# Kernel tuning notes

Measured on AMD Instinct MI355X. Metric: run time of the kernel, lower is better.

## Reference

```python
import jax, jax.numpy as jnp
import numpy as np

B, N, D, H = 4, 2048, 512, 8
KD = D // H  # per-head key/value dim = 64
NORM = 1.0 / np.sqrt(KD).astype(np.float32)


def setup_inputs() -> dict:
    key = jax.random.key(0)
    kq, km, k1, k2, k3 = jax.random.split(key, 5)
    s = 1.0 / np.sqrt(D)
    return {
        "queries": jax.random.normal(kq, (B, N, D), dtype=jnp.float32),
        "mask": jax.random.randint(km, (B, N, N), 0, 2).astype(jnp.bool_),
        "Wq": jax.random.normal(k1, (D, D), dtype=jnp.float32) * s,
        "Wk": jax.random.normal(k2, (D, D), dtype=jnp.float32) * s,
        "Wc": jax.random.normal(k3, (D, D), dtype=jnp.float32) * s,
    }


def reference(queries, mask, Wq, Wk, Wc):
    # Self-attention path (keys=None, values=None): V uses key_embed (Wk).
    Q = (queries @ Wq.T).reshape(B, N, H, KD)  # [B,N,H,kd]
    K = (queries @ Wk.T).reshape(B, N, H, KD)
    V = K  # original code: V = key_embed(queries) when values is None
    scores = NORM * jnp.einsum("bqhd,bkhd->bhqk", Q, K)  # [B,H,N,N]
    scores = jnp.where(mask[:, None, :, :], -jnp.inf, scores)
    attn = jax.nn.softmax(scores, axis=-1)
    out = jnp.einsum("bhqk,bkhd->bqhd", attn, V).reshape(B, N, H * KD)
    return out @ Wc.T  # [B,N,D]
```

## Files before the change

kernel.cpp:

```cpp
#include <hip/hip_runtime.h>
#include <hip/hip_bf16.h>
#include <math.h>

#define B_ 4
#define N_ 2048
#define D_ 512
#define H_ 8
#define NORM2_ 0.18033688011112042f

typedef __attribute__((ext_vector_type(8))) short short8;
typedef __attribute__((ext_vector_type(4))) float f32x4;
#define MFMA16(a, b, c) __builtin_amdgcn_mfma_f32_16x16x32_bf16(a, b, c, 0, 0, 0)
#define EXP2(x) __builtin_amdgcn_exp2f(x)

static __device__ __forceinline__ uint32_t pk2(float lo, float hi) {
  __hip_bfloat162 h = __float22bfloat162_rn(make_float2(lo, hi));
  return *(reinterpret_cast<uint32_t*>(&h));
}

static __device__ __forceinline__ void async16(const ushort* lds, const ushort* g) {
  __builtin_amdgcn_global_load_lds(
      (const __attribute__((address_space(1))) uint32_t*)g,
      (__attribute__((address_space(3))) uint32_t*)(ushort*)lds, 16, 0, 0);
}

__global__ __launch_bounds__(256) void prep(const float* __restrict__ q,
                                            const int* __restrict__ mask,
                                            const float* __restrict__ wq,
                                            const float* __restrict__ wk,
                                            const float* __restrict__ wc,
                                            ushort* __restrict__ Xb,
                                            ushort* __restrict__ Wb,
                                            uint32_t* __restrict__ pk) {
  const int bx = blockIdx.x;
  if (bx < 2048) {
    const int lane = threadIdx.x & 63;
    const int wid = ((bx << 8) + threadIdx.x) >> 6;
    for (int i = wid; i < 65536; i += 8192) {
      const int4 m = ((const int4*)mask)[(size_t)i * 64 + lane];
      uint32_t nib = (uint32_t)(m.x != 0) | ((uint32_t)(m.y != 0) << 1) |
                     ((uint32_t)(m.z != 0) << 2) | ((uint32_t)(m.w != 0) << 3);
      nib |= __shfl_xor(nib, 1) << 4;
      nib |= __shfl_xor(nib, 2) << 8;
      nib |= __shfl_xor(nib, 4) << 16;
      if ((lane & 7) == 0) pk[i * 8 + (lane >> 3)] = nib;
    }
  } else if (bx < 3072) {
    const int i = ((bx - 2048) << 8) + threadIdx.x;
    for (int j = i; j < 1048576; j += 262144) {
      const float4 v = ((const float4*)q)[j];
      uint2 o; o.x = pk2(v.x, v.y); o.y = pk2(v.z, v.w);
      ((uint2*)Xb)[j] = o;
    }
  } else {
    const int i = ((bx - 3072) << 8) + threadIdx.x;
    for (int j = i; j < 196608; j += 24576) {
      const int wi = j >> 16, off = j & 65535;
      const float* src = (wi == 0) ? wq : (wi == 1) ? wk : wc;
      const float4 v = ((const float4*)src)[off];
      uint2 o; o.x = pk2(v.x, v.y); o.y = pk2(v.z, v.w);
      ((uint2*)Wb)[j] = o;
    }
  }
}

__global__ __launch_bounds__(256) void merge(const ushort* __restrict__ P0,
                                             const float* __restrict__ l0,
                                             const float* __restrict__ l1,
                                             ushort* __restrict__ Ab) {
  const int j = (blockIdx.x << 8) + threadIdx.x;
  const int h = (j >> 3) & 7;
  const int tok = j >> 6;
  const int b = tok >> 11, n = tok & 2047;
  const int li = ((b * H_ + h) << 11) + n;
  const float inv = 1.f / (l0[li] + l1[li]);
  const uint4 a0 = ((const uint4*)P0)[j];
  const uint4 a1 = ((const uint4*)Ab)[j];
  uint4 o;
  const uint32_t* u0 = (const uint32_t*)&a0;
  const uint32_t* u1 = (const uint32_t*)&a1;
  uint32_t* uo = (uint32_t*)&o;
#pragma unroll
  for (int m = 0; m < 4; ++m) {
    const float lo = __uint_as_float(u0[m] << 16) + __uint_as_float(u1[m] << 16);
    const float hi = __uint_as_float(u0[m] & 0xFFFF0000u) +
                     __uint_as_float(u1[m] & 0xFFFF0000u);
    uo[m] = pk2(lo * inv, hi * inv);
  }
  ((uint4*)Ab)[j] = o;
}

template <int F32OUT>
__global__ __launch_bounds__(256) void gemm128(const ushort* __restrict__ X,
                                               const ushort* __restrict__ W0,
                                               const ushort* __restrict__ W1,
                                               void* __restrict__ C0,
                                               void* __restrict__ C1,
                                               float s0, float s1) {
  const ushort* Wp = (blockIdx.z == 0) ? W0 : W1;
  void* Cp = (blockIdx.z == 0) ? C0 : C1;
  const float sc = (blockIdx.z == 0) ? s0 : s1;
  const int t = threadIdx.x;
  const int w = t >> 6, lane = t & 63, quad = lane >> 4, c = lane & 15;
  const int wm = w & 1, wn = w >> 1;
  const int n0 = blockIdx.x * 128, m0 = blockIdx.y * 128;
  __shared__ __align__(16) ushort Xs[2][128][64];
  __shared__ __align__(16) ushort Ws[2][128][64];
  f32x4 acc[4][4];
#pragma unroll
  for (int i = 0; i < 4; ++i)
#pragma unroll
    for (int j = 0; j < 4; ++j) acc[i][j] = (f32x4){0.f, 0.f, 0.f, 0.f};

#define GSTAGE(bf, k0)                                                        \
  do {                                                                        \
    _Pragma("unroll") for (int g = 0; g < 4; ++g) {                           \
      const int id = w * 256 + g * 64 + lane;                                 \
      const int row = id >> 3, lch = id & 7;                                  \
      const int gch = lch ^ (row & 7);                                        \
      async16(&Xs[bf][row][lch * 8], X + (size_t)(m0 + row) * D_ + (k0) + gch * 8); \
      async16(&Ws[bf][row][lch * 8], Wp + (size_t)(n0 + row) * D_ + (k0) + gch * 8); \
    }                                                                         \
  } while (0)

  GSTAGE(0, 0);
  __syncthreads();
  const int NK = D_ / 64;
  for (int kt = 0; kt < NK; ++kt) {
    const int bf = kt & 1;
    if (kt + 1 < NK) GSTAGE(bf ^ 1, (kt + 1) * 64);
#pragma unroll
    for (int s = 0; s < 2; ++s) {
      short8 af[4], bt[4];
#pragma unroll
      for (int i = 0; i < 4; ++i) {
        const int rA = wn * 64 + i * 16 + c;
        af[i] = *(const short8*)&Ws[bf][rA][(((s * 4 + quad) ^ (rA & 7)) & 7) * 8];
        const int rB = wm * 64 + i * 16 + c;
        bt[i] = *(const short8*)&Xs[bf][rB][(((s * 4 + quad) ^ (rB & 7)) & 7) * 8];
      }
#pragma unroll
      for (int i = 0; i < 4; ++i)
#pragma unroll
        for (int j = 0; j < 4; ++j) acc[i][j] = MFMA16(af[i], bt[j], acc[i][j]);
    }
    if (kt + 1 < NK) __syncthreads();
  }
#undef GSTAGE
#pragma unroll
  for (int i = 0; i < 4; ++i)
#pragma unroll
    for (int j = 0; j < 4; ++j) {
      const size_t off =
          (size_t)(m0 + wm * 64 + j * 16 + c) * D_ + n0 + wn * 64 + i * 16 + quad * 4;
      if (F32OUT) {
        float4 v; v.x = acc[i][j][0]; v.y = acc[i][j][1]; v.z = acc[i][j][2]; v.w = acc[i][j][3];
        *(float4*)((float*)Cp + off) = v;
      } else {
        uint2 uv;
        uv.x = pk2(acc[i][j][0] * sc, acc[i][j][1] * sc);
        uv.y = pk2(acc[i][j][2] * sc, acc[i][j][3] * sc);
        *(uint2*)((ushort*)Cp + off) = uv;
      }
    }
}

__global__ __launch_bounds__(256) void attn_mfma(const ushort* __restrict__ Qb,
                                                 const ushort* __restrict__ Kb,
                                                 const uint32_t* __restrict__ pk,
                                                 ushort* __restrict__ P0,
                                                 ushort* __restrict__ P1,
                                                 float* __restrict__ l0,
                                                 float* __restrict__ l1) {
  const int qt64 = blockIdx.x >> 1, hf = blockIdx.x & 1;
  const int h = blockIdx.y, b = blockIdx.z;
  const int q0 = qt64 * 64;
  const int t = threadIdx.x;
  const int w = t >> 6, lane = t & 63, quad = lane >> 4, c = lane & 15;

  __shared__ __align__(16) ushort Ks[64][64];
  __shared__ __align__(16) uint32_t KtU[64][32];
  __shared__ __align__(16) ushort QP[4][16][72];
  ushort(*Qs)[64] = (ushort(*)[64]) & QP[0][0][0];
  ushort(*Pq)[16][72] = QP;

#pragma unroll
  for (int p = 0; p < 2; ++p) {
    const int id = t + p * 256;
    const int row = id >> 3, lch = id & 7, gch = lch ^ (row & 7);
    async16(&Qs[row][lch * 8], Qb + (size_t)(b * N_ + q0 + row) * D_ + h * 64 + gch * 8);
  }
  __syncthreads();
  const int rq = (w << 4) + c;
  const short8 bq0 = *(const short8*)&Qs[rq][((quad ^ (rq & 7)) & 7) * 8];
  const short8 bq1 = *(const short8*)&Qs[rq][(((4 + quad) ^ (rq & 7)) & 7) * 8];

  short8 vones;
#pragma unroll
  for (int i = 0; i < 8; ++i) vones[i] = (short)0x3F80;

  f32x4 o[4];
#pragma unroll
  for (int i = 0; i < 4; ++i) o[i] = (f32x4){0.f, 0.f, 0.f, 0.f};
  f32x4 o5 = (f32x4){0.f, 0.f, 0.f, 0.f};

  const int kp = t >> 3, ch = t & 7;
  const int r0 = 2 * kp, r1 = r0 + 1;
  const int ksw0 = ((ch ^ (r0 & 7)) & 7) * 8, ksw1 = ((ch ^ (r1 & 7)) & 7) * 8;
  const ushort* kb0 =
      Kb + (size_t)(b * N_ + hf * 1024 + 2 * kp) * D_ + h * 64 + ch * 8;
  const uint32_t* pkq =
      pk + ((size_t)(b * N_ + q0 + (w << 4) + c) << 6) + hf * 32;

  uint4 c0 = *(const uint4*)kb0;
  uint4 c1 = *(const uint4*)(kb0 + D_);
  uint2 cm = *(const uint2*)pkq;
  uint4 nx0, nx1; uint2 nxm;

  const int NT = 16;
  for (int kt = 0; kt < NT; ++kt) {
    __syncthreads();
    *(uint4*)&Ks[r0][ksw0] = c0;
    *(uint4*)&Ks[r1][ksw1] = c1;
    const uint32_t* a0 = (const uint32_t*)&c0;
    const uint32_t* a1 = (const uint32_t*)&c1;
#pragma unroll
    for (int m = 0; m < 4; ++m) {
      const uint32_t lo = __builtin_amdgcn_perm(a1[m], a0[m], 0x05040100);
      const uint32_t hi = __builtin_amdgcn_perm(a1[m], a0[m], 0x07060302);
      const int j0 = 2 * m, j1 = 2 * m + 1;
      KtU[ch * 8 + j0][(kp & 3) | ((((kp >> 2) ^ j0 ^ ch) & 7) << 2)] = lo;
      KtU[ch * 8 + j1][(kp & 3) | ((((kp >> 2) ^ j1 ^ ch) & 7) << 2)] = hi;
    }
    __syncthreads();

    if (kt + 1 < NT) {
      const ushort* kbn = kb0 + (size_t)(kt + 1) * 64 * D_;
      nx0 = *(const uint4*)kbn;
      nx1 = *(const uint4*)(kbn + D_);
      nxm = *(const uint2*)(pkq + (kt + 1) * 2);
    }

#pragma unroll
    for (int tI = 0; tI < 4; ++tI) {
      const int rk = tI * 16 + c;
      const short8 aK0 = *(const short8*)&Ks[rk][((quad ^ (rk & 7)) & 7) * 8];
      const short8 aK1 = *(const short8*)&Ks[rk][(((4 + quad) ^ (rk & 7)) & 7) * 8];
      f32x4 z = (f32x4){0.f, 0.f, 0.f, 0.f};
      z = MFMA16(aK0, bq0, z);
      z = MFMA16(aK1, bq1, z);
      const uint32_t mw = (tI < 2) ? cm.x : cm.y;
      const int bb = ((tI & 1) << 4) + quad * 4;
      uint32_t pb[4];
#pragma unroll
      for (int r = 0; r < 4; ++r) {
        const float e = EXP2(z[r]);
        pb[r] = ((mw >> (bb + r)) & 1u) ? 0u : __float_as_uint(e);
      }
      const uint32_t pw0 = __builtin_amdgcn_perm(pb[1], pb[0], 0x07060302);
      const uint32_t pw1 = __builtin_amdgcn_perm(pb[3], pb[2], 0x07060302);
      *(uint2*)&Pq[w][c][tI * 16 + quad * 4] = make_uint2(pw0, pw1);
    }

    const short8 bp0 = *(const short8*)&Pq[w][c][quad * 8];
    const short8 bp1 = *(const short8*)&Pq[w][c][32 + quad * 8];
    o5 = MFMA16(vones, bp0, o5);
    o5 = MFMA16(vones, bp1, o5);
#pragma unroll
    for (int dt = 0; dt < 4; ++dt) {
      const int dd = dt * 16 + c;
      const int g = (c & 7) ^ ((2 * dt + (c >> 3)) & 7);
      const short8 aV0 = *(const short8*)&KtU[dd][((quad ^ g) & 7) << 2];
      const short8 aV1 = *(const short8*)&KtU[dd][(((4 + quad) ^ g) & 7) << 2];
      o[dt] = MFMA16(aV0, bp0, o[dt]);
      o[dt] = MFMA16(aV1, bp1, o[dt]);
    }

    if (kt + 1 < NT) { c0 = nx0; c1 = nx1; cm = nxm; }
  }

  ushort* Pp = hf ? P1 : P0;
  float* lp = hf ? l1 : l0;
#pragma unroll
  for (int dt = 0; dt < 4; ++dt) {
    uint2 uv;
    uv.x = pk2(o[dt][0], o[dt][1]);
    uv.y = pk2(o[dt][2], o[dt][3]);
    *(uint2*)(Pp + (size_t)(b * N_ + q0 + (w << 4) + c) * D_ + h * 64 + dt * 16 + quad * 4) = uv;
  }
  if (quad == 0) lp[((b * H_ + h) << 11) + q0 + (w << 4) + c] = o5[0];
}

extern "C" void kernel_launch(void* const* d_in, const int* in_sizes, int n_in,
                              void* d_out, int out_size, void* d_ws, size_t ws_size,
                              hipStream_t stream) {
  const float* queries = (const float*)d_in[0];
  const int* mask = (const int*)d_in[1];
  const float* Wq = (const float*)d_in[2];
  const float* Wk = (const float*)d_in[3];
  const float* Wc = (const float*)d_in[4];
  float* out = (float*)d_out;

  const size_t nTok = (size_t)B_ * N_;
  const size_t nXD = nTok * D_;
  const size_t nW = (size_t)D_ * D_;
  ushort* Xb = (ushort*)d_ws;
  ushort* Wqb = Xb + nXD;
  ushort* Wkb = Wqb + nW;
  ushort* Wcb = Wkb + nW;
  ushort* Qb = Wcb + nW;
  ushort* Kb = Qb + nXD;
  ushort* Ab = Kb + nXD;
  uint32_t* pk = (uint32_t*)(Ab + nXD);
  ushort* P0 = Xb;
  ushort* P1 = Ab;
  float* l0 = (float*)Wqb;
  float* l1 = (float*)Wkb;

  prep<<<3168, 256, 0, stream>>>(queries, mask, Wq, Wk, Wc, Xb, Wqb, pk);
  gemm128<0><<<dim3(D_ / 128, (int)(nTok / 128), 2), 256, 0, stream>>>(
      Xb, Wqb, Wkb, Qb, Kb, NORM2_, 1.0f);
  attn_mfma<<<dim3(64, H_, B_), 256, 0, stream>>>(Qb, Kb, pk, P0, P1, l0, l1);
  merge<<<2048, 256, 0, stream>>>(P0, l0, l1, Ab);
  gemm128<1><<<dim3(D_ / 128, (int)(nTok / 128), 1), 256, 0, stream>>>(
      Ab, Wcb, nullptr, out, nullptr, 1.0f, 1.0f);
}
```

Measured before the change: 209.6 us.

## Split attention warps 2x2 over query and key halves with LDS reduction

Changes the warp decomposition in the attention kernel so each warp handles 32 query rows and 32 of the 64 keys in each tile, instead of 16 query rows and all 64 keys. Each K/V fragment read from LDS now feeds two MFMAs, which cuts LDS reads per MFMA. Partial outputs from the two key-half warps are summed through shared memory at the end. Row sums are written per key half into an extended l buffer, and merge adds all four parts. This costs more accumulator registers and an extra reduction with two barriers, and it needs the l buffers to have room for the extra 65536 entries.

```diff
diff --git a/kernel.cpp b/kernel.cpp
--- a/kernel.cpp
+++ b/kernel.cpp
@@ -73,7 +73,8 @@
   const int tok = j >> 6;
   const int b = tok >> 11, n = tok & 2047;
   const int li = ((b * H_ + h) << 11) + n;
-  const float inv = 1.f / (l0[li] + l1[li]);
+  const float inv =
+      1.f / (l0[li] + l0[65536 + li] + l1[li] + l1[65536 + li]);
   const uint4 a0 = ((const uint4*)P0)[j];
   const uint4 a1 = ((const uint4*)Ab)[j];
   uint4 o;
@@ -177,12 +178,14 @@
   const int q0 = qt64 * 64;
   const int t = threadIdx.x;
   const int w = t >> 6, lane = t & 63, quad = lane >> 4, c = lane & 15;
+  const int wq = w & 1, wk = w >> 1;
 
   __shared__ __align__(16) ushort Ks[64][64];
   __shared__ __align__(16) uint32_t KtU[64][32];
-  __shared__ __align__(16) ushort QP[4][16][72];
-  ushort(*Qs)[64] = (ushort(*)[64]) & QP[0][0][0];
-  ushort(*Pq)[16][72] = QP;
+  __shared__ __align__(16) unsigned char U[16896];
+  ushort(*Qs)[64] = (ushort(*)[64])U;
+  ushort(*PqN)[32][40] = (ushort(*)[32][40])U;
+  float* Ored = (float*)U;
 
 #pragma unroll
   for (int p = 0; p < 2; ++p) {
@@ -191,31 +194,40 @@
     async16(&Qs[row][lch * 8], Qb + (size_t)(b * N_ + q0 + row) * D_ + h * 64 + gch * 8);
   }
   __syncthreads();
-  const int rq = (w << 4) + c;
-  const short8 bq0 = *(const short8*)&Qs[rq][((quad ^ (rq & 7)) & 7) * 8];
-  const short8 bq1 = *(const short8*)&Qs[rq][(((4 + quad) ^ (rq & 7)) & 7) * 8];
+  short8 bq0[2], bq1[2];
+#pragma unroll
+  for (int sq = 0; sq < 2; ++sq) {
+    const int rq = wq * 32 + sq * 16 + c;
+    bq0[sq] = *(const short8*)&Qs[rq][((quad ^ (rq & 7)) & 7) * 8];
+    bq1[sq] = *(const short8*)&Qs[rq][(((4 + quad) ^ (rq & 7)) & 7) * 8];
+  }
 
   short8 vones;
 #pragma unroll
   for (int i = 0; i < 8; ++i) vones[i] = (short)0x3F80;
 
-  f32x4 o[4];
-#pragma unroll
-  for (int i = 0; i < 4; ++i) o[i] = (f32x4){0.f, 0.f, 0.f, 0.f};
-  f32x4 o5 = (f32x4){0.f, 0.f, 0.f, 0.f};
+  f32x4 o[4][2];
+#pragma unroll
+  for (int i = 0; i < 4; ++i)
+#pragma unroll
+    for (int sq = 0; sq < 2; ++sq) o[i][sq] = (f32x4){0.f, 0.f, 0.f, 0.f};
+  f32x4 o5[2];
+  o5[0] = (f32x4){0.f, 0.f, 0.f, 0.f};
+  o5[1] = (f32x4){0.f, 0.f, 0.f, 0.f};
 
   const int kp = t >> 3, ch = t & 7;
   const int r0 = 2 * kp, r1 = r0 + 1;
   const int ksw0 = ((ch ^ (r0 & 7)) & 7) * 8, ksw1 = ((ch ^ (r1 & 7)) & 7) * 8;
   const ushort* kb0 =
       Kb + (size_t)(b * N_ + hf * 1024 + 2 * kp) * D_ + h * 64 + ch * 8;
-  const uint32_t* pkq =
-      pk + ((size_t)(b * N_ + q0 + (w << 4) + c) << 6) + hf * 32;
+  const uint32_t* pkq0 =
+      pk + ((size_t)(b * N_ + q0 + wq * 32 + c) << 6) + hf * 32 + wk;
+  const uint32_t* pkq1 = pkq0 + (16 << 6);
 
   uint4 c0 = *(const uint4*)kb0;
   uint4 c1 = *(const uint4*)(kb0 + D_);
-  uint2 cm = *(const uint2*)pkq;
-  uint4 nx0, nx1; uint2 nxm;
+  uint32_t cm0 = pkq0[0], cm1 = pkq1[0];
+  uint4 nx0, nx1; uint32_t nxm0, nxm1;
 
   const int NT = 16;
   for (int kt = 0; kt < NT; ++kt) {
@@ -238,57 +250,87 @@
       const ushort* kbn = kb0 + (size_t)(kt + 1) * 64 * D_;
       nx0 = *(const uint4*)kbn;
       nx1 = *(const uint4*)(kbn + D_);
-      nxm = *(const uint2*)(pkq + (kt + 1) * 2);
-    }
-
-#pragma unroll
-    for (int tI = 0; tI < 4; ++tI) {
-      const int rk = tI * 16 + c;
+      nxm0 = pkq0[(kt + 1) * 2];
+      nxm1 = pkq1[(kt + 1) * 2];
+    }
+
+#pragma unroll
+    for (int tK = 0; tK < 2; ++tK) {
+      const int rk = wk * 32 + tK * 16 + c;
       const short8 aK0 = *(const short8*)&Ks[rk][((quad ^ (rk & 7)) & 7) * 8];
       const short8 aK1 = *(const short8*)&Ks[rk][(((4 + quad) ^ (rk & 7)) & 7) * 8];
-      f32x4 z = (f32x4){0.f, 0.f, 0.f, 0.f};
-      z = MFMA16(aK0, bq0, z);
-      z = MFMA16(aK1, bq1, z);
-      const uint32_t mw = (tI < 2) ? cm.x : cm.y;
-      const int bb = ((tI & 1) << 4) + quad * 4;
-      uint32_t pb[4];
-#pragma unroll
-      for (int r = 0; r < 4; ++r) {
-        const float e = EXP2(z[r]);
-        pb[r] = ((mw >> (bb + r)) & 1u) ? 0u : __float_as_uint(e);
+#pragma unroll
+      for (int sq = 0; sq < 2; ++sq) {
+        f32x4 z = (f32x4){0.f, 0.f, 0.f, 0.f};
+        z = MFMA16(aK0, bq0[sq], z);
+        z = MFMA16(aK1, bq1[sq], z);
+        const uint32_t mw = sq ? cm1 : cm0;
+        const int bb = tK * 16 + quad * 4;
+        uint32_t pb[4];
+#pragma unroll
+        for (int r = 0; r < 4; ++r) {
+          const float e = EXP2(z[r]);
+          pb[r] = ((mw >> (bb + r)) & 1u) ? 0u : __float_as_uint(e);
+        }
+        const uint32_t pw0 = __builtin_amdgcn_perm(pb[1], pb[0], 0x07060302);
+        const uint32_t pw1 = __builtin_amdgcn_perm(pb[3], pb[2], 0x07060302);
+        *(uint2*)&PqN[w][sq * 16 + c][tK * 16 + quad * 4] = make_uint2(pw0, pw1);
       }
-      const uint32_t pw0 = __builtin_amdgcn_perm(pb[1], pb[0], 0x07060302);
-      const uint32_t pw1 = __builtin_amdgcn_perm(pb[3], pb[2], 0x07060302);
-      *(uint2*)&Pq[w][c][tI * 16 + quad * 4] = make_uint2(pw0, pw1);
-    }
-
-    const short8 bp0 = *(const short8*)&Pq[w][c][quad * 8];
-    const short8 bp1 = *(const short8*)&Pq[w][c][32 + quad * 8];
-    o5 = MFMA16(vones, bp0, o5);
-    o5 = MFMA16(vones, bp1, o5);
+    }
+
+    const short8 bp0 = *(const short8*)&PqN[w][c][quad * 8];
+    const short8 bp1 = *(const short8*)&PqN[w][16 + c][quad * 8];
+    o5[0] = MFMA16(vones, bp0, o5[0]);
+    o5[1] = MFMA16(vones, bp1, o5[1]);
 #pragma unroll
     for (int dt = 0; dt < 4; ++dt) {
       const int dd = dt * 16 + c;
-      const int g = (c & 7) ^ ((2 * dt + (c >> 3)) & 7);
-      const short8 aV0 = *(const short8*)&KtU[dd][((quad ^ g) & 7) << 2];
-      const short8 aV1 = *(const short8*)&KtU[dd][(((4 + quad) ^ g) & 7) << 2];
-      o[dt] = MFMA16(aV0, bp0, o[dt]);
-      o[dt] = MFMA16(aV1, bp1, o[dt]);
-    }
-
-    if (kt + 1 < NT) { c0 = nx0; c1 = nx1; cm = nxm; }
-  }
-
-  ushort* Pp = hf ? P1 : P0;
+      const int g2 = (((wk << 2) + quad) ^ (c & 7) ^ ((2 * dt + (c >> 3)) & 7)) & 7;
+      const short8 aV = *(const short8*)&KtU[dd][g2 << 2];
+      o[dt][0] = MFMA16(aV, bp0, o[dt][0]);
+      o[dt][1] = MFMA16(aV, bp1, o[dt][1]);
+    }
+
+    if (kt + 1 < NT) { c0 = nx0; c1 = nx1; cm0 = nxm0; cm1 = nxm1; }
+  }
+
   float* lp = hf ? l1 : l0;
-#pragma unroll
-  for (int dt = 0; dt < 4; ++dt) {
-    uint2 uv;
-    uv.x = pk2(o[dt][0], o[dt][1]);
-    uv.y = pk2(o[dt][2], o[dt][3]);
-    *(uint2*)(Pp + (size_t)(b * N_ + q0 + (w << 4) + c) * D_ + h * 64 + dt * 16 + quad * 4) = uv;
-  }
-  if (quad == 0) lp[((b * H_ + h) << 11) + q0 + (w << 4) + c] = o5[0];
+  if (quad == 0) {
+#pragma unroll
+    for (int sq = 0; sq < 2; ++sq)
+      lp[wk * 65536 + ((b * H_ + h) << 11) + q0 + wq * 32 + sq * 16 + c] = o5[sq][0];
+  }
+
+  __syncthreads();
+  if (wk == 0) {
+#pragma unroll
+    for (int dt = 0; dt < 4; ++dt)
+#pragma unroll
+      for (int sq = 0; sq < 2; ++sq)
+#pragma unroll
+        for (int jj = 0; jj < 4; ++jj)
+          Ored[wq * 2112 + (dt * 16 + quad * 4 + jj) * 33 + sq * 16 + c] =
+              o[dt][sq][jj];
+  }
+  __syncthreads();
+  if (wk == 1) {
+    ushort* Pp = hf ? P1 : P0;
+#pragma unroll
+    for (int dt = 0; dt < 4; ++dt)
+#pragma unroll
+      for (int sq = 0; sq < 2; ++sq) {
+        float r[4];
+#pragma unroll
+        for (int jj = 0; jj < 4; ++jj)
+          r[jj] = o[dt][sq][jj] +
+                  Ored[wq * 2112 + (dt * 16 + quad * 4 + jj) * 33 + sq * 16 + c];
+        uint2 uv;
+        uv.x = pk2(r[0], r[1]);
+        uv.y = pk2(r[2], r[3]);
+        *(uint2*)(Pp + (size_t)(b * N_ + q0 + wq * 32 + sq * 16 + c) * D_ + h * 64 +
+                  dt * 16 + quad * 4) = uv;
+      }
+  }
 }
 
 extern "C" void kernel_launch(void* const* d_in, const int* in_sizes, int n_in,
```

Result: slower. 214.9 us (+2.5%).
